# Performance work log

Measured on AMD Instinct MI355X. Metric: run time of the kernel, lower is better.

Reference implementation:

```python
import jax, jax.numpy as jnp
import numpy as np

D_MODEL = 1024
N_HEADS = 16
D_K = D_MODEL // N_HEADS


def setup_inputs() -> dict:
    key = jax.random.key(0)
    ks = jax.random.split(key, 9)
    s = 1.0 / np.sqrt(D_MODEL)
    def lin(kw, kb):
        W = jax.random.uniform(kw, (D_MODEL, D_MODEL), jnp.float32, -s, s)
        b = jax.random.uniform(kb, (D_MODEL,), jnp.float32, -s, s)
        return W, b
    wq, bq = lin(ks[0], ks[1])
    wk, bk = lin(ks[2], ks[3])
    wv, bv = lin(ks[4], ks[5])
    wo, bo = lin(ks[6], ks[7])
    x = jax.random.normal(ks[8], (2, 2048, D_MODEL), jnp.float32)
    return {"x": x, "wq": wq, "bq": bq, "wk": wk, "bk": bk,
            "wv": wv, "bv": bv, "wo": wo, "bo": bo}


def reference(x, wq, bq, wk, bk, wv, bv, wo, bo):
    B, S, D = x.shape
    scale = 1.0 / np.sqrt(D_K)
    # projections (torch Linear: y = x W^T + b); W stored as [in,out] here
    q = x @ wq + bq
    k = x @ wk + bk
    v = x @ wv + bv
    # [B, H, S, d_k]
    q = q.reshape(B, S, N_HEADS, D_K).transpose(0, 2, 1, 3)
    k = k.reshape(B, S, N_HEADS, D_K).transpose(0, 2, 1, 3)
    v = v.reshape(B, S, N_HEADS, D_K).transpose(0, 2, 1, 3)
    scores = jnp.einsum('bhqd,bhkd->bhqk', q, k) * scale
    attn = jax.nn.softmax(scores, axis=-1)
    out = jnp.einsum('bhqk,bhkd->bhqd', attn, v)
    out = out.transpose(0, 2, 1, 3).reshape(B, S, D)
    return out @ wo + bo
```

## Files before the change

### kernel.cpp

```cpp
#include <hip/hip_runtime.h>
#include <hip/hip_bf16.h>
#include <math.h>

typedef __bf16 bf16x8 __attribute__((ext_vector_type(8)));
typedef unsigned short u16x8 __attribute__((ext_vector_type(8)));
typedef unsigned short u16x4 __attribute__((ext_vector_type(4)));
typedef float f32x4 __attribute__((ext_vector_type(4)));
typedef unsigned int u32x4 __attribute__((ext_vector_type(4)));
typedef unsigned int u32x2 __attribute__((ext_vector_type(2)));
typedef unsigned short u16;

__device__ __forceinline__ u16 f2bf(float f) {
    unsigned int x = __float_as_uint(f);
    x += 0x7fffu + ((x >> 16) & 1u);
    return (u16)(x >> 16);
}
__device__ __forceinline__ void glds16(const void* g, void* l) {
    __builtin_amdgcn_global_load_lds(
        (const __attribute__((address_space(1))) void*)g,
        (__attribute__((address_space(3))) void*)l, 16, 0, 0);
}
__device__ __forceinline__ void swap_half(unsigned& a, unsigned& b) {
    u32x2 t = __builtin_amdgcn_permlane32_swap(a, b, false, false);
    t = __builtin_amdgcn_permlane16_swap(t[0], t[1], false, false);
    a = t[0]; b = t[1];
}

__global__ __launch_bounds__(256) void prep(const float* __restrict__ W0, const float* __restrict__ W1,
                                            const float* __restrict__ W2, const float* __restrict__ W3,
                                            const float* __restrict__ X,
                                            u16* __restrict__ Wt, u16* __restrict__ Xb) {
    int z = blockIdx.z;
    if (z >= 4) {
        int row = (z - 4) * 1024 + blockIdx.y * 32 + blockIdx.x;
        const float* src = X + (size_t)row * 1024 + threadIdx.x * 4;
        f32x4 v = *(const f32x4*)src;
        u16x4 o; o[0] = f2bf(v[0]); o[1] = f2bf(v[1]); o[2] = f2bf(v[2]); o[3] = f2bf(v[3]);
        *(u16x4*)&Xb[(size_t)row * 1024 + threadIdx.x * 4] = o;
        return;
    }
    __shared__ float T[32][33];
    const float* W = (z == 0) ? W0 : ((z == 1) ? W1 : ((z == 2) ? W2 : W3));
    u16* dst = Wt + (size_t)z * 1024 * 1024;
    int k0 = blockIdx.y * 32, n0 = blockIdx.x * 32;
    int x = threadIdx.x & 31, y0 = threadIdx.x >> 5;
#pragma unroll
    for (int i = 0; i < 4; i++) {
        int y = y0 + i * 8;
        T[y][x] = W[(size_t)(k0 + y) * 1024 + n0 + x];
    }
    __syncthreads();
#pragma unroll
    for (int i = 0; i < 4; i++) {
        int y = y0 + i * 8;
        dst[(size_t)(n0 + y) * 1024 + k0 + x] = f2bf(T[x][y]);
    }
}

template <bool OF32, bool VSPLIT>
__global__ __launch_bounds__(256) void gemm(
    const u16* __restrict__ Bt,
    const float* __restrict__ b0, const float* __restrict__ b1, const float* __restrict__ b2,
    const u16* __restrict__ A, void* __restrict__ Cptr, u16* __restrict__ Vt, int Ntot)
{
    __shared__ __align__(16) u16 As[128 * 32];
    __shared__ __align__(16) u16 Bs[128 * 32];
    int tid = threadIdx.x;
    int lane = tid & 63, l15 = lane & 15, quad = lane >> 4;
    int wid = tid >> 6, wm = wid >> 1, wn = wid & 1;
    int m0 = blockIdx.y * 128, n0 = blockIdx.x * 128;
    int sel = n0 >> 10;
    const float* bias = (sel == 0) ? b0 : ((sel == 1) ? b1 : b2);

    f32x4 acc[4][4];
#pragma unroll
    for (int i = 0; i < 4; i++)
#pragma unroll
        for (int j = 0; j < 4; j++) { f32x4 z = {0.f, 0.f, 0.f, 0.f}; acc[i][j] = z; }

    int rr = lane >> 2;
    int cc = (lane & 3) ^ ((rr >> 1) & 3);
    const u16* abase = A  + (size_t)m0 * 1024;
    const u16* bbase = Bt + (size_t)n0 * 1024;
    int fsw = (l15 >> 1) & 3;

    for (int k0 = 0; k0 < 1024; k0 += 32) {
#pragma unroll
        for (int inst = 0; inst < 2; inst++) {
            int r0 = wid * 32 + inst * 16;
            glds16(&abase[(size_t)(r0 + rr) * 1024 + k0 + cc * 8], &As[r0 * 32]);
            glds16(&bbase[(size_t)(r0 + rr) * 1024 + k0 + cc * 8], &Bs[r0 * 32]);
        }
        __syncthreads();
        bf16x8 af[4], bf[4];
#pragma unroll
        for (int mt = 0; mt < 4; mt++)
            af[mt] = *(const bf16x8*)&As[(wm * 64 + mt * 16 + l15) * 32 + ((quad ^ fsw) * 8)];
#pragma unroll
        for (int nt = 0; nt < 4; nt++)
            bf[nt] = *(const bf16x8*)&Bs[(wn * 64 + nt * 16 + l15) * 32 + ((quad ^ fsw) * 8)];
#pragma unroll
        for (int mt = 0; mt < 4; mt++)
#pragma unroll
            for (int nt = 0; nt < 4; nt++)
                acc[mt][nt] = __builtin_amdgcn_mfma_f32_16x16x32_bf16(af[mt], bf[nt], acc[mt][nt], 0, 0, 0);
        __syncthreads();
    }
    if (VSPLIT && sel == 2) {
        int b = m0 >> 11;
#pragma unroll
        for (int mt = 0; mt < 4; mt++) {
            int gr = m0 + wm * 64 + mt * 16 + quad * 4;
            int s = gr & 2047;
#pragma unroll
            for (int nt = 0; nt < 4; nt++) {
                int gcl = (n0 & 1023) + wn * 64 + nt * 16 + l15;
                float bb = bias[gcl];
                u16x4 pk;
#pragma unroll
                for (int r = 0; r < 4; r++) pk[r] = f2bf(acc[mt][nt][r] + bb);
                *(u16x4*)&Vt[(size_t)((b * 16 + (gcl >> 6)) * 64 + (gcl & 63)) * 2048 + s] = pk;
            }
        }
        return;
    }
    float qs = (VSPLIT && sel == 0) ? 0.18033688011112f : 1.0f;
#pragma unroll
    for (int mt = 0; mt < 4; mt++) {
        int gr = m0 + wm * 64 + mt * 16 + quad * 4;
#pragma unroll
        for (int nt = 0; nt < 4; nt++) {
            int gc = n0 + wn * 64 + nt * 16 + l15;
            float bb = bias[gc & 1023];
#pragma unroll
            for (int r = 0; r < 4; r++) {
                float v = (acc[mt][nt][r] + bb) * qs;
                if (OF32) ((float*)Cptr)[(size_t)(gr + r) * Ntot + gc] = v;
                else      ((u16*)Cptr)[(size_t)(gr + r) * Ntot + gc] = f2bf(v);
            }
        }
    }
}

__global__ __launch_bounds__(256, 2) void attn(const u16* __restrict__ QKV,
                                               const u16* __restrict__ Vt,
                                               u16* __restrict__ O)
{
    __shared__ __align__(16) u16 Ks[2][64 * 64];
    __shared__ __align__(16) u16 Vs[2][64 * 64];
    const int S = 2048, DQ = 3072;
    int tid = threadIdx.x, wid = tid >> 6, lane = tid & 63;
    int l15 = lane & 15, quad = lane >> 4;
    int qt = blockIdx.x, h = blockIdx.y, b = blockIdx.z;
    const u16* base = QKV + (size_t)b * S * DQ + h * 64;
    const u16* Kb = base + 1024;
    const u16* Vtb = Vt + (size_t)((b * 16 + h) * 64) * 2048;
    int q0 = qt * 128 + wid * 32;

    bf16x8 qA0 = *(const bf16x8*)&base[(size_t)(q0 + l15) * DQ + quad * 8];
    bf16x8 qA1 = *(const bf16x8*)&base[(size_t)(q0 + l15) * DQ + 32 + quad * 8];
    bf16x8 qB0 = *(const bf16x8*)&base[(size_t)(q0 + 16 + l15) * DQ + quad * 8];
    bf16x8 qB1 = *(const bf16x8*)&base[(size_t)(q0 + 16 + l15) * DQ + 32 + quad * 8];

    f32x4 oA[4], oB[4];
#pragma unroll
    for (int i = 0; i < 4; i++) { f32x4 z = {0.f, 0.f, 0.f, 0.f}; oA[i] = z; oB[i] = z; }
    float psA = 0.f, psB = 0.f;

    int rr = lane >> 3;
    int cc = (lane & 7) ^ rr;
    int fs7 = l15 & 7;

    auto stage = [&](int it, int bsel) {
        int kv0 = it << 6;
#pragma unroll
        for (int inst = 0; inst < 2; inst++) {
            int r0 = wid * 16 + inst * 8;
            glds16(&Kb[(size_t)(kv0 + r0 + rr) * DQ + cc * 8], &Ks[bsel][r0 * 64]);
            glds16(&Vtb[(size_t)(r0 + rr) * 2048 + kv0 + cc * 8], &Vs[bsel][r0 * 64]);
        }
    };

    stage(0, 0);
#pragma unroll 2
    for (int it = 0; it < 32; ++it) {
        int cur = it & 1;
        if (it < 31) {
            stage(it + 1, cur ^ 1);
            asm volatile("s_waitcnt vmcnt(4)\n\ts_barrier" ::: "memory");
        } else {
            asm volatile("s_waitcnt vmcnt(0)\n\ts_barrier" ::: "memory");
        }

        f32x4 sA[4], sB[4];
#pragma unroll
        for (int t = 0; t < 4; t++) { f32x4 z = {0.f, 0.f, 0.f, 0.f}; sA[t] = z; sB[t] = z; }
#pragma unroll
        for (int t = 0; t < 4; t++) {
            bf16x8 kfa = *(const bf16x8*)&Ks[cur][(t * 16 + l15) * 64 + ((quad ^ fs7) * 8)];
            bf16x8 kfb = *(const bf16x8*)&Ks[cur][(t * 16 + l15) * 64 + (((quad + 4) ^ fs7) * 8)];
            sA[t] = __builtin_amdgcn_mfma_f32_16x16x32_bf16(kfa, qA0, sA[t], 0, 0, 0);
            sA[t] = __builtin_amdgcn_mfma_f32_16x16x32_bf16(kfb, qA1, sA[t], 0, 0, 0);
            sB[t] = __builtin_amdgcn_mfma_f32_16x16x32_bf16(kfa, qB0, sB[t], 0, 0, 0);
            sB[t] = __builtin_amdgcn_mfma_f32_16x16x32_bf16(kfb, qB1, sB[t], 0, 0, 0);
        }

        unsigned wA[4][2], wB[4][2];
#pragma unroll
        for (int t = 0; t < 4; t++) {
            float a0 = __builtin_amdgcn_exp2f(sA[t][0]);
            float a1 = __builtin_amdgcn_exp2f(sA[t][1]);
            float a2 = __builtin_amdgcn_exp2f(sA[t][2]);
            float a3 = __builtin_amdgcn_exp2f(sA[t][3]);
            psA += (a0 + a1) + (a2 + a3);
            asm("v_cvt_pk_bf16_f32 %0, %1, %2" : "=v"(wA[t][0]) : "v"(a0), "v"(a1));
            asm("v_cvt_pk_bf16_f32 %0, %1, %2" : "=v"(wA[t][1]) : "v"(a2), "v"(a3));
            float b0_ = __builtin_amdgcn_exp2f(sB[t][0]);
            float b1_ = __builtin_amdgcn_exp2f(sB[t][1]);
            float b2_ = __builtin_amdgcn_exp2f(sB[t][2]);
            float b3_ = __builtin_amdgcn_exp2f(sB[t][3]);
            psB += (b0_ + b1_) + (b2_ + b3_);
            asm("v_cvt_pk_bf16_f32 %0, %1, %2" : "=v"(wB[t][0]) : "v"(b0_), "v"(b1_));
            asm("v_cvt_pk_bf16_f32 %0, %1, %2" : "=v"(wB[t][1]) : "v"(b2_), "v"(b3_));
        }
        unsigned a0 = wA[0][0], a2 = wA[1][0]; swap_half(a0, a2);
        unsigned a1 = wA[0][1], a3 = wA[1][1]; swap_half(a1, a3);
        unsigned c0 = wA[2][0], c2 = wA[3][0]; swap_half(c0, c2);
        unsigned c1 = wA[2][1], c3 = wA[3][1]; swap_half(c1, c3);
        u32x4 pdA0 = {a0, a1, a2, a3};
        u32x4 pdA1 = {c0, c1, c2, c3};
        bf16x8 pfA0 = *(bf16x8*)&pdA0;
        bf16x8 pfA1 = *(bf16x8*)&pdA1;
        unsigned d0 = wB[0][0], d2 = wB[1][0]; swap_half(d0, d2);
        unsigned d1 = wB[0][1], d3 = wB[1][1]; swap_half(d1, d3);
        unsigned e0 = wB[2][0], e2 = wB[3][0]; swap_half(e0, e2);
        unsigned e1 = wB[2][1], e3 = wB[3][1]; swap_half(e1, e3);
        u32x4 pdB0 = {d0, d1, d2, d3};
        u32x4 pdB1 = {e0, e1, e2, e3};
        bf16x8 pfB0 = *(bf16x8*)&pdB0;
        bf16x8 pfB1 = *(bf16x8*)&pdB1;

#pragma unroll
        for (int dt = 0; dt < 4; dt++) {
            bf16x8 vfa = *(const bf16x8*)&Vs[cur][(dt * 16 + l15) * 64 + ((quad ^ fs7) * 8)];
            bf16x8 vfb = *(const bf16x8*)&Vs[cur][(dt * 16 + l15) * 64 + (((quad + 4) ^ fs7) * 8)];
            oA[dt] = __builtin_amdgcn_mfma_f32_16x16x32_bf16(pfA0, vfa, oA[dt], 0, 0, 0);
            oA[dt] = __builtin_amdgcn_mfma_f32_16x16x32_bf16(pfA1, vfb, oA[dt], 0, 0, 0);
            oB[dt] = __builtin_amdgcn_mfma_f32_16x16x32_bf16(pfB0, vfa, oB[dt], 0, 0, 0);
            oB[dt] = __builtin_amdgcn_mfma_f32_16x16x32_bf16(pfB1, vfb, oB[dt], 0, 0, 0);
        }
        asm volatile("s_barrier" ::: "memory");
    }

    psA += __shfl_xor(psA, 16);
    psA += __shfl_xor(psA, 32);
    psB += __shfl_xor(psB, 16);
    psB += __shfl_xor(psB, 32);
#pragma unroll
    for (int r = 0; r < 4; r++) {
        float invA = 1.0f / __shfl(psA, quad * 4 + r);
        size_t rowA = (size_t)(b * S + q0 + quad * 4 + r);
#pragma unroll
        for (int dt = 0; dt < 4; dt++)
            O[rowA * 1024 + h * 64 + dt * 16 + l15] = f2bf(oA[dt][r] * invA);
        float invB = 1.0f / __shfl(psB, quad * 4 + r);
        size_t rowB = rowA + 16;
#pragma unroll
        for (int dt = 0; dt < 4; dt++)
            O[rowB * 1024 + h * 64 + dt * 16 + l15] = f2bf(oB[dt][r] * invB);
    }
}

extern "C" void kernel_launch(void* const* d_in, const int* in_sizes, int n_in,
                              void* d_out, int out_size, void* d_ws, size_t ws_size,
                              hipStream_t stream) {
    const float* x  = (const float*)d_in[0];
    const float* wq = (const float*)d_in[1];
    const float* bq = (const float*)d_in[2];
    const float* wk = (const float*)d_in[3];
    const float* bk = (const float*)d_in[4];
    const float* wv = (const float*)d_in[5];
    const float* bv = (const float*)d_in[6];
    const float* wo = (const float*)d_in[7];
    const float* bo = (const float*)d_in[8];
    float* out = (float*)d_out;

    u16* qkv  = (u16*)d_ws;
    u16* obuf = qkv  + (size_t)4096 * 3072;
    u16* vt   = obuf + (size_t)4096 * 1024;
    u16* wt   = vt   + (size_t)2048 * 2048;
    u16* xb   = wt   + (size_t)4 * 1024 * 1024;

    dim3 tb(256);
    prep<<<dim3(32, 32, 8), tb, 0, stream>>>(wq, wk, wv, wo, x, wt, xb);
    gemm<false, true><<<dim3(24, 32), tb, 0, stream>>>(wt, bq, bk, bv, xb, qkv, vt, 3072);
    attn<<<dim3(16, 16, 2), tb, 0, stream>>>(qkv, vt, obuf);
    gemm<true, false><<<dim3(8, 32), tb, 0, stream>>>(wt + (size_t)3 * 1024 * 1024,
                                                      bo, bo, bo, obuf, out, (u16*)nullptr, 1024);
}
```

Baseline: 203.0 us.

## Add 256x256 double-buffered LDS GEMM kernel for the QKV projection

Replaces the 128x128-tile QKV projection GEMM with a new 512-thread kernel that uses 256x256 output tiles and a K step of 64. It double-buffers A and B in LDS through direct global-to-LDS loads with an XOR swizzle. Loads for the next K step are interleaved with MFMA phases, and s_setprio is raised around the MFMA blocks. The larger tile cuts global traffic per FLOP and overlaps loads with compute. The trade-off is that only 192 blocks launch, fewer than the CU count, and at about 128KB of LDS per block, occupancy is one block per CU.

```diff
diff --git a/kernel.cpp b/kernel.cpp
--- a/kernel.cpp
+++ b/kernel.cpp
@@ -54,6 +54,147 @@
     for (int i = 0; i < 4; i++) {
         int y = y0 + i * 8;
         dst[(size_t)(n0 + y) * 1024 + k0 + x] = f2bf(T[x][y]);
+    }
+}
+
+__global__ __launch_bounds__(512, 2) void gemm256(
+    const u16* __restrict__ Bt,
+    const float* __restrict__ b0, const float* __restrict__ b1, const float* __restrict__ b2,
+    const u16* __restrict__ A, u16* __restrict__ C, u16* __restrict__ Vt)
+{
+    __shared__ __align__(16) u16 As[2][256 * 64];
+    __shared__ __align__(16) u16 Bs[2][256 * 64];
+    int tid = threadIdx.x;
+    int lane = tid & 63, l15 = lane & 15, quad = lane >> 4;
+    int wid = tid >> 6;
+    int wm = wid >> 2, wn = wid & 3;
+    int m0 = blockIdx.y * 256, n0 = blockIdx.x * 256;
+    int sel = n0 >> 10;
+    const float* bias = (sel == 0) ? b0 : ((sel == 1) ? b1 : b2);
+
+    f32x4 acc[8][4];
+#pragma unroll
+    for (int i = 0; i < 8; i++)
+#pragma unroll
+        for (int j = 0; j < 4; j++) { f32x4 z = {0.f, 0.f, 0.f, 0.f}; acc[i][j] = z; }
+
+    int rr = lane >> 3;
+    int cc = (lane & 7) ^ rr;
+    int fs7 = l15 & 7;
+    const u16* abase = A  + (size_t)m0 * 1024;
+    const u16* bbase = Bt + (size_t)n0 * 1024;
+
+    auto stage = [&](int kt, int hp, int buf) {
+        const u16* gsrc = (hp < 2) ? abase : bbase;
+        u16* ldst = (hp < 2) ? As[buf] : Bs[buf];
+        int k0 = kt * 64;
+        int hbase = (hp & 1) * 128;
+#pragma unroll
+        for (int inst = 0; inst < 2; inst++) {
+            int r0 = hbase + wid * 16 + inst * 8;
+            glds16(&gsrc[(size_t)(r0 + rr) * 1024 + k0 + cc * 8], &ldst[r0 * 64]);
+        }
+    };
+
+#pragma unroll
+    for (int hp = 0; hp < 4; hp++) stage(0, hp, 0);
+
+#pragma unroll 2
+    for (int it = 0; it < 16; ++it) {
+        int c = it & 1;
+        if (it < 15) {
+            stage(it + 1, 0, c ^ 1);
+            asm volatile("s_waitcnt vmcnt(2)");
+        } else {
+            asm volatile("s_waitcnt vmcnt(0)");
+        }
+        __builtin_amdgcn_s_barrier();
+        bf16x8 bfr[4][2];
+#pragma unroll
+        for (int nt = 0; nt < 4; nt++)
+#pragma unroll
+            for (int h = 0; h < 2; h++)
+                bfr[nt][h] = *(const bf16x8*)&Bs[c][(wn * 64 + nt * 16 + l15) * 64 +
+                                                    ((((h << 2) | quad) ^ fs7) * 8)];
+        {
+            bf16x8 af[2][2];
+#pragma unroll
+            for (int m = 0; m < 2; m++)
+#pragma unroll
+                for (int h = 0; h < 2; h++)
+                    af[m][h] = *(const bf16x8*)&As[c][(wm * 128 + m * 16 + l15) * 64 +
+                                                      ((((h << 2) | quad) ^ fs7) * 8)];
+            asm volatile("s_waitcnt lgkmcnt(0)");
+            __builtin_amdgcn_sched_barrier(0);
+            __builtin_amdgcn_s_setprio(1);
+#pragma unroll
+            for (int m = 0; m < 2; m++)
+#pragma unroll
+                for (int nt = 0; nt < 4; nt++)
+#pragma unroll
+                    for (int h = 0; h < 2; h++)
+                        acc[m][nt] = __builtin_amdgcn_mfma_f32_16x16x32_bf16(
+                            af[m][h], bfr[nt][h], acc[m][nt], 0, 0, 0);
+            __builtin_amdgcn_s_setprio(0);
+            __builtin_amdgcn_s_barrier();
+        }
+#pragma unroll
+        for (int p = 1; p < 4; p++) {
+            bf16x8 af[2][2];
+#pragma unroll
+            for (int m = 0; m < 2; m++)
+#pragma unroll
+                for (int h = 0; h < 2; h++)
+                    af[m][h] = *(const bf16x8*)&As[c][(wm * 128 + (p * 2 + m) * 16 + l15) * 64 +
+                                                      ((((h << 2) | quad) ^ fs7) * 8)];
+            if (it < 15) stage(it + 1, p, c ^ 1);
+            __builtin_amdgcn_s_barrier();
+            asm volatile("s_waitcnt lgkmcnt(0)");
+            __builtin_amdgcn_sched_barrier(0);
+            __builtin_amdgcn_s_setprio(1);
+#pragma unroll
+            for (int m = 0; m < 2; m++)
+#pragma unroll
+                for (int nt = 0; nt < 4; nt++)
+#pragma unroll
+                    for (int h = 0; h < 2; h++)
+                        acc[p * 2 + m][nt] = __builtin_amdgcn_mfma_f32_16x16x32_bf16(
+                            af[m][h], bfr[nt][h], acc[p * 2 + m][nt], 0, 0, 0);
+            __builtin_amdgcn_s_setprio(0);
+            __builtin_amdgcn_s_barrier();
+        }
+    }
+
+    if (sel == 2) {
+        int b = m0 >> 11;
+#pragma unroll
+        for (int mt = 0; mt < 8; mt++) {
+            int gr = m0 + wm * 128 + mt * 16 + quad * 4;
+            int s = gr & 2047;
+#pragma unroll
+            for (int nt = 0; nt < 4; nt++) {
+                int gcl = (n0 & 1023) + wn * 64 + nt * 16 + l15;
+                float bb = bias[gcl];
+                u16x4 pk;
+#pragma unroll
+                for (int r = 0; r < 4; r++) pk[r] = f2bf(acc[mt][nt][r] + bb);
+                *(u16x4*)&Vt[(size_t)((b * 16 + (gcl >> 6)) * 64 + (gcl & 63)) * 2048 + s] = pk;
+            }
+        }
+        return;
+    }
+    float qs = (sel == 0) ? 0.18033688011112f : 1.0f;
+#pragma unroll
+    for (int mt = 0; mt < 8; mt++) {
+        int gr = m0 + wm * 128 + mt * 16 + quad * 4;
+#pragma unroll
+        for (int nt = 0; nt < 4; nt++) {
+            int gc = n0 + wn * 64 + nt * 16 + l15;
+            float bb = bias[gc & 1023];
+#pragma unroll
+            for (int r = 0; r < 4; r++)
+                C[(size_t)(gr + r) * 3072 + gc] = f2bf((acc[mt][nt][r] + bb) * qs);
+        }
     }
 }
 
@@ -293,7 +434,7 @@
 
     dim3 tb(256);
     prep<<<dim3(32, 32, 8), tb, 0, stream>>>(wq, wk, wv, wo, x, wt, xb);
-    gemm<false, true><<<dim3(24, 32), tb, 0, stream>>>(wt, bq, bk, bv, xb, qkv, vt, 3072);
+    gemm256<<<dim3(12, 16), dim3(512), 0, stream>>>(wt, bq, bk, bv, xb, qkv, vt);
     attn<<<dim3(16, 16, 2), tb, 0, stream>>>(qkv, vt, obuf);
     gemm<true, false><<<dim3(8, 32), tb, 0, stream>>>(wt + (size_t)3 * 1024 * 1024,
                                                       bo, bo, bo, obuf, out, (u16*)nullptr, 1024);
```

Result: faster. 195.0 us (-3.9%).
